# Performance work log

Measured on AMD Instinct MI355X. Metric: run time of the kernel, lower is better.

## Reference

```python
import jax, jax.numpy as jnp
import numpy as np


def l2norm(x, axis=-1, eps=1e-06):
    inv_norm = jax.lax.rsqrt(jnp.sum(x * x, axis=axis, keepdims=True) + eps)
    return x * inv_norm


def setup_inputs() -> dict:
    key0 = jax.random.key(0)
    ks = jax.random.split(key0, 5)
    B, S, H, Dk, Dv = 4, 2048, 16, 128, 128
    query = jax.random.normal(ks[0], (B, S, H, Dk), dtype=jnp.float32)
    key = jax.random.normal(ks[1], (B, S, H, Dk), dtype=jnp.float32)
    value = jax.random.normal(ks[2], (B, S, H, Dv), dtype=jnp.float32)
    # g is a log-decay: negative so decay = exp(g) in (exp(-1), 1)
    g = -jax.random.uniform(ks[3], (B, S, H), dtype=jnp.float32)
    # beta plays the role of sigmoid(.) mixing coefficient in (0, 1)
    beta = jax.random.uniform(ks[4], (B, S, H), dtype=jnp.float32)
    return {"query": query, "key": key, "value": value, "g": g, "beta": beta}


def reference(query, key, value, g, beta):
    # Gated delta-rule recurrence (Qwen3.5 GatedDeltaNet / recurrent_gated_delta_rule)
    dtype = query.dtype
    q = l2norm(query)
    k = l2norm(key)
    v = value
    scale = 1.0 / float(np.sqrt(q.shape[-1]))
    q = q * scale
    # time-major: [S, B, H, D]
    q = jnp.swapaxes(q, 0, 1)
    k = jnp.swapaxes(k, 0, 1)
    v = jnp.swapaxes(v, 0, 1)
    g_t = jnp.swapaxes(g, 0, 1)
    b_t = jnp.swapaxes(beta, 0, 1)
    B, H, Dk = q.shape[1], q.shape[2], q.shape[3]
    Dv = v.shape[3]
    init_state = jnp.zeros((B, H, Dk, Dv), dtype=dtype)

    def step_fn(state, inputs):
        q_i, k_i, v_i, g_i, beta_i = inputs
        decay = jnp.exp(g_i)[..., None, None]            # [B,H,1,1]
        state = state * decay                            # [B,H,Dk,Dv]
        kv_mem = jnp.sum(state * k_i[..., :, None], axis=-2)   # [B,H,Dv]
        delta = (v_i - kv_mem) * beta_i[..., None]              # [B,H,Dv]
        state = state + k_i[..., :, None] * delta[..., None, :]
        out_i = jnp.sum(state * q_i[..., :, None], axis=-2)    # [B,H,Dv]
        return state, out_i

    final_state, outputs = jax.lax.scan(step_fn, init_state, (q, k, v, g_t, b_t))
    outputs = jnp.swapaxes(outputs, 0, 1).astype(dtype)  # [B,S,H,Dv]
    return outputs, final_state.astype(dtype)
```

## Files before the change

kernel.cpp:

```cpp
#include <hip/hip_runtime.h>


#define Bsz 4
#define Ssz 2048
#define Hsz 16
#define Dsz 128

constexpr int ROWS = Bsz * Ssz * Hsz;
constexpr int VSTR = Hsz * Dsz;
constexpr float EPS = 1e-6f;
constexpr float SCALE = 0.08838834764831845f;

typedef float v2f __attribute__((ext_vector_type(2)));

template <int CTRL>
__device__ __forceinline__ float dpp_add(float x) {
  int y = __builtin_amdgcn_update_dpp(0, __float_as_int(x), CTRL, 0xF, 0xF, true);
  return x + __int_as_float(y);
}
__device__ __forceinline__ float reduce16(float x) {
  x = dpp_add<0xB1>(x);
  x = dpp_add<0x4E>(x);
  x = dpp_add<0x141>(x);
  x = dpp_add<0x140>(x);
  return x;
}

__global__ __launch_bounds__(256) void prep_kernel(
    const float* __restrict__ q, const float* __restrict__ k,
    const float* __restrict__ g, const float* __restrict__ beta,
    float4* __restrict__ pack) {
  int wid = threadIdx.x >> 6;
  int lane = threadIdx.x & 63;
  int lg = lane & 15;
  int rg = lane >> 4;
  int r = blockIdx.x * 16 + wid * 4 + rg;
  const float4* qp = reinterpret_cast<const float4*>(q + (size_t)r * Dsz);
  const float4* kp = reinterpret_cast<const float4*>(k + (size_t)r * Dsz);
  float4 qa = qp[lg * 2], qb = qp[lg * 2 + 1];
  float4 ka = kp[lg * 2], kb = kp[lg * 2 + 1];
  float sq = qa.x * qa.x + qa.y * qa.y + qa.z * qa.z + qa.w * qa.w +
             qb.x * qb.x + qb.y * qb.y + qb.z * qb.z + qb.w * qb.w;
  float sk = ka.x * ka.x + ka.y * ka.y + ka.z * ka.z + ka.w * ka.w +
             kb.x * kb.x + kb.y * kb.y + kb.z * kb.z + kb.w * kb.w;
  sq = reduce16(sq);
  sk = reduce16(sk);
  if (lg == 0) {
    float xq = sq + EPS;
    float rq = rsqrtf(xq);
    rq = rq * (1.5f - 0.5f * xq * rq * rq);
    float xk = sk + EPS;
    float rk = rsqrtf(xk);
    rk = rk * (1.5f - 0.5f * xk * rk * rk);
    float dec = expf(g[r]);
    float bi = beta[r] * rk;
    int h = r % Hsz;
    int s = (r / Hsz) % Ssz;
    int b = r / (Hsz * Ssz);
    pack[(size_t)(b * Hsz + h) * Ssz + s] = make_float4(dec, rk, rq * SCALE, bi);
  }
}

#define DDEPTH 8
#define BATCH 4
#define SLOT_B 1280
#define WAVE_B (DDEPTH * SLOT_B)

__device__ __forceinline__ void dma16(unsigned long long g, unsigned int l) {
  __builtin_amdgcn_global_load_lds(
      (const __attribute__((address_space(1))) void*)g,
      (__attribute__((address_space(3))) void*)(unsigned long long)l, 16, 0, 0);
}
__device__ __forceinline__ void dma4(unsigned long long g, unsigned int l) {
  __builtin_amdgcn_global_load_lds(
      (const __attribute__((address_space(1))) void*)g,
      (__attribute__((address_space(3))) void*)(unsigned long long)l, 4, 0, 0);
}

struct BufP {
  v2f kr[4];
  v2f qr[4];
  float4 p;
  float vv;
};

__device__ __forceinline__ void ld_buf(BufP& b, const char* slot, int dkl, int dvg) {
  const float4* kp = (const float4*)(slot + dkl * 16);
  float4 k0 = kp[0];
  float4 k1 = kp[16];
  float4 q0 = kp[32];
  float4 q1 = kp[48];
  b.kr[0] = (v2f){k0.x, k0.y};
  b.kr[1] = (v2f){k0.z, k0.w};
  b.kr[2] = (v2f){k1.x, k1.y};
  b.kr[3] = (v2f){k1.z, k1.w};
  b.qr[0] = (v2f){q0.x, q0.y};
  b.qr[1] = (v2f){q0.z, q0.w};
  b.qr[2] = (v2f){q1.x, q1.y};
  b.qr[3] = (v2f){q1.z, q1.w};
  b.vv = *(const float*)(slot + 1024 + dvg * 4);
  b.p = *(const float4*)(slot + 1040);
}

__device__ __forceinline__ float step_compute(const BufP& b, v2f (&st)[4]) {
  v2f a0 = st[0] * b.kr[0];
  v2f a1 = st[1] * b.kr[1];
  a0 = __builtin_elementwise_fma(st[2], b.kr[2], a0);
  a1 = __builtin_elementwise_fma(st[3], b.kr[3], a1);
  float acc = (a0.x + a0.y) + (a1.x + a1.y);
  acc = reduce16(acc);
  float dec = b.p.x;
  float kv = acc * dec * b.p.y;
  float dl = (b.vv - kv) * b.p.w;
  v2f dec2 = (v2f){dec, dec};
  v2f dl2 = (v2f){dl, dl};
  v2f o0 = (v2f){0.f, 0.f};
  v2f o1 = (v2f){0.f, 0.f};
#pragma unroll
  for (int i = 0; i < 4; i += 2) {
    st[i] = __builtin_elementwise_fma(st[i], dec2, b.kr[i] * dl2);
    st[i + 1] = __builtin_elementwise_fma(st[i + 1], dec2, b.kr[i + 1] * dl2);
    o0 = __builtin_elementwise_fma(st[i], b.qr[i], o0);
    o1 = __builtin_elementwise_fma(st[i + 1], b.qr[i + 1], o1);
  }
  float oacc = (o0.x + o0.y) + (o1.x + o1.y);
  oacc = reduce16(oacc);
  return oacc * b.p.z;
}

__global__ __launch_bounds__(256, 2) void scan_kernel(
    const float* __restrict__ q, const float* __restrict__ k,
    const float* __restrict__ v, const float4* __restrict__ pack,
    float* __restrict__ out, float* __restrict__ stateOut) {
  __shared__ __align__(16) char smem[4 * WAVE_B];

  const int blk = blockIdx.x;
  const int bh = blk & 63;
  const int cc = blk >> 6;
  const int tid = threadIdx.x;
  const int lane = tid & 63;
  const int wid = __builtin_amdgcn_readfirstlane(tid >> 6);
  const int dkl = lane & 15;
  const int dvg = lane >> 4;
  const int dv = cc * 16 + wid * 4 + dvg;

  const size_t base = ((size_t)(bh >> 4) * Ssz * Hsz + (bh & 15)) * Dsz;
  const float4* pp = pack + (size_t)bh * Ssz;

  const unsigned int wb3 =
      (unsigned int)(unsigned long long)(void*)smem + (unsigned int)(wid * WAVE_B);
  const char* wbg = smem + wid * WAVE_B;

  const int li = lane & 31;
  const int fofs = (li < 16) ? (8 * li) : (8 * (li - 16) + 4);
  unsigned long long kq_g =
      (unsigned long long)(uintptr_t)(((lane < 32) ? k : q) + base + fofs);
  unsigned long long vp_g;
  unsigned int vp_stride;
  if (lane < 4) {
    vp_g = (unsigned long long)(uintptr_t)(v + base + cc * 16 + wid * 4 + lane);
    vp_stride = VSTR * 4;
  } else {
    int pc = (lane < 8) ? (lane - 4) : 0;
    vp_g = (unsigned long long)(uintptr_t)((const float*)pp + pc);
    vp_stride = 16;
  }

#pragma unroll
  for (int r = 0; r < DDEPTH; ++r) {
    dma16(kq_g, wb3 + r * SLOT_B);
    dma4(vp_g, wb3 + r * SLOT_B + 1024);
    kq_g += VSTR * 4;
    vp_g += vp_stride;
  }
  int nrow = DDEPTH;

  v2f st[4];
#pragma unroll
  for (int i = 0; i < 4; ++i) st[i] = (v2f){0.f, 0.f};

  float* outp = out + base + (size_t)dkl * VSTR + dv;
  float ocap = 0.f;
  BufP A, Bb;

  for (int sb = 0; sb < Ssz; sb += 16) {
#pragma unroll
    for (int gg = 0; gg < 4; ++gg) {
      const int s0 = (gg & 1) * BATCH;
      asm volatile("s_waitcnt vmcnt(8)" ::: "memory");
      ld_buf(A, wbg + (s0 + 0) * SLOT_B, dkl, dvg);
      __builtin_amdgcn_sched_barrier(0);
      ld_buf(Bb, wbg + (s0 + 1) * SLOT_B, dkl, dvg);
      __builtin_amdgcn_sched_barrier(0);
      {
        float o = step_compute(A, st);
        ocap = (dkl == gg * 4 + 0) ? o : ocap;
      }
      ld_buf(A, wbg + (s0 + 2) * SLOT_B, dkl, dvg);
      __builtin_amdgcn_sched_barrier(0);
      {
        float o = step_compute(Bb, st);
        ocap = (dkl == gg * 4 + 1) ? o : ocap;
      }
      ld_buf(Bb, wbg + (s0 + 3) * SLOT_B, dkl, dvg);
      __builtin_amdgcn_sched_barrier(0);
      {
        float o = step_compute(A, st);
        ocap = (dkl == gg * 4 + 2) ? o : ocap;
      }
      {
        float o = step_compute(Bb, st);
        ocap = (dkl == gg * 4 + 3) ? o : ocap;
      }
      if (gg == 3) {
        *outp = ocap;
        outp += 16 * VSTR;
      }
      asm volatile("s_waitcnt lgkmcnt(0)" ::: "memory");
#pragma unroll
      for (int j = 0; j < BATCH; ++j) {
        dma16(kq_g, wb3 + (s0 + j) * SLOT_B);
        dma4(vp_g, wb3 + (s0 + j) * SLOT_B + 1024);
        if (nrow < Ssz - 1) {
          kq_g += VSTR * 4;
          vp_g += vp_stride;
          ++nrow;
        }
      }
    }
  }

  float* sp = stateOut + ((size_t)bh * Dsz + dkl * 8) * Dsz + dv;
#pragma unroll
  for (int j = 0; j < 4; ++j) {
    sp[(2 * j) * Dsz] = st[j].x;
    sp[(2 * j + 1) * Dsz] = st[j].y;
  }
}

extern "C" void kernel_launch(void* const* d_in, const int* in_sizes, int n_in,
                              void* d_out, int out_size, void* d_ws, size_t ws_size,
                              hipStream_t stream) {
  const float* q = (const float*)d_in[0];
  const float* k = (const float*)d_in[1];
  const float* v = (const float*)d_in[2];
  const float* g = (const float*)d_in[3];
  const float* beta = (const float*)d_in[4];
  float* out = (float*)d_out;
  float* stateOut = out + (size_t)Bsz * Ssz * Hsz * Dsz;
  float4* pack = (float4*)d_ws;

  prep_kernel<<<ROWS / 16, 256, 0, stream>>>(q, k, g, beta, pack);
  scan_kernel<<<512, 256, 0, stream>>>(q, k, v, pack, out, stateOut);
}
```

Measured before the change: 717.7 us.

## Split state across 32 lanes per column and double scan blocks

Each wave now covers 2 value columns with 32 lanes per column instead of 4 columns with 16 lanes, so every lane holds 4 state elements instead of 8. The grid grows to 1024 blocks with occupancy hint 4, and the LDS slot shrinks. Reductions gain a ds_swizzle step across 32 lanes, and only 8 lanes issue the v/pack DMA. The aim is to shorten the per-step serial chain and raise parallelism, at the cost of an extra cross-lane step per reduction and double the k/q staging traffic per column.

```diff
diff --git a/kernel.cpp b/kernel.cpp
--- a/kernel.cpp
+++ b/kernel.cpp
@@ -24,6 +24,11 @@
   x = dpp_add<0x141>(x);
   x = dpp_add<0x140>(x);
   return x;
+}
+__device__ __forceinline__ float reduce32(float x) {
+  x = reduce16(x);
+  int y = __builtin_amdgcn_ds_swizzle(__float_as_int(x), 0x401F);
+  return x + __int_as_float(y);
 }
 
 __global__ __launch_bounds__(256) void prep_kernel(
@@ -63,7 +68,7 @@
 
 #define DDEPTH 8
 #define BATCH 4
-#define SLOT_B 1280
+#define SLOT_B 1056
 #define WAVE_B (DDEPTH * SLOT_B)
 
 __device__ __forceinline__ void dma16(unsigned long long g, unsigned int l) {
@@ -77,58 +82,42 @@
       (__attribute__((address_space(3))) void*)(unsigned long long)l, 4, 0, 0);
 }
 
-struct BufP {
-  v2f kr[4];
-  v2f qr[4];
+struct Buf2 {
+  v2f kr0, kr1, qr0, qr1;
   float4 p;
   float vv;
 };
 
-__device__ __forceinline__ void ld_buf(BufP& b, const char* slot, int dkl, int dvg) {
-  const float4* kp = (const float4*)(slot + dkl * 16);
-  float4 k0 = kp[0];
-  float4 k1 = kp[16];
-  float4 q0 = kp[32];
-  float4 q1 = kp[48];
-  b.kr[0] = (v2f){k0.x, k0.y};
-  b.kr[1] = (v2f){k0.z, k0.w};
-  b.kr[2] = (v2f){k1.x, k1.y};
-  b.kr[3] = (v2f){k1.z, k1.w};
-  b.qr[0] = (v2f){q0.x, q0.y};
-  b.qr[1] = (v2f){q0.z, q0.w};
-  b.qr[2] = (v2f){q1.x, q1.y};
-  b.qr[3] = (v2f){q1.z, q1.w};
-  b.vv = *(const float*)(slot + 1024 + dvg * 4);
+__device__ __forceinline__ void ld_buf2(Buf2& b, const char* slot, int dkl, int dvg) {
+  const float* sf = (const float*)slot;
+  b.kr0 = (v2f){sf[dkl], sf[dkl + 32]};
+  b.kr1 = (v2f){sf[dkl + 64], sf[dkl + 96]};
+  b.qr0 = (v2f){sf[128 + dkl], sf[128 + dkl + 32]};
+  b.qr1 = (v2f){sf[128 + dkl + 64], sf[128 + dkl + 96]};
+  b.vv = sf[256 + dvg];
   b.p = *(const float4*)(slot + 1040);
 }
 
-__device__ __forceinline__ float step_compute(const BufP& b, v2f (&st)[4]) {
-  v2f a0 = st[0] * b.kr[0];
-  v2f a1 = st[1] * b.kr[1];
-  a0 = __builtin_elementwise_fma(st[2], b.kr[2], a0);
-  a1 = __builtin_elementwise_fma(st[3], b.kr[3], a1);
-  float acc = (a0.x + a0.y) + (a1.x + a1.y);
-  acc = reduce16(acc);
+__device__ __forceinline__ float step_compute2(const Buf2& b, v2f (&st)[2]) {
+  v2f a = st[0] * b.kr0;
+  a = __builtin_elementwise_fma(st[1], b.kr1, a);
+  float acc = a.x + a.y;
+  acc = reduce32(acc);
   float dec = b.p.x;
   float kv = acc * dec * b.p.y;
   float dl = (b.vv - kv) * b.p.w;
   v2f dec2 = (v2f){dec, dec};
   v2f dl2 = (v2f){dl, dl};
-  v2f o0 = (v2f){0.f, 0.f};
-  v2f o1 = (v2f){0.f, 0.f};
-#pragma unroll
-  for (int i = 0; i < 4; i += 2) {
-    st[i] = __builtin_elementwise_fma(st[i], dec2, b.kr[i] * dl2);
-    st[i + 1] = __builtin_elementwise_fma(st[i + 1], dec2, b.kr[i + 1] * dl2);
-    o0 = __builtin_elementwise_fma(st[i], b.qr[i], o0);
-    o1 = __builtin_elementwise_fma(st[i + 1], b.qr[i + 1], o1);
-  }
-  float oacc = (o0.x + o0.y) + (o1.x + o1.y);
-  oacc = reduce16(oacc);
+  st[0] = __builtin_elementwise_fma(st[0], dec2, b.kr0 * dl2);
+  st[1] = __builtin_elementwise_fma(st[1], dec2, b.kr1 * dl2);
+  v2f o = st[0] * b.qr0;
+  o = __builtin_elementwise_fma(st[1], b.qr1, o);
+  float oacc = o.x + o.y;
+  oacc = reduce32(oacc);
   return oacc * b.p.z;
 }
 
-__global__ __launch_bounds__(256, 2) void scan_kernel(
+__global__ __launch_bounds__(256, 4) void scan_kernel(
     const float* __restrict__ q, const float* __restrict__ k,
     const float* __restrict__ v, const float4* __restrict__ pack,
     float* __restrict__ out, float* __restrict__ stateOut) {
@@ -140,9 +129,10 @@
   const int tid = threadIdx.x;
   const int lane = tid & 63;
   const int wid = __builtin_amdgcn_readfirstlane(tid >> 6);
-  const int dkl = lane & 15;
-  const int dvg = lane >> 4;
-  const int dv = cc * 16 + wid * 4 + dvg;
+  const int dkl = lane & 31;
+  const int dvg = lane >> 5;
+  const int dv0 = cc * 8 + wid * 2;
+  const int dv = dv0 + dvg;
 
   const size_t base = ((size_t)(bh >> 4) * Ssz * Hsz + (bh & 15)) * Dsz;
   const float4* pp = pack + (size_t)bh * Ssz;
@@ -152,16 +142,15 @@
   const char* wbg = smem + wid * WAVE_B;
 
   const int li = lane & 31;
-  const int fofs = (li < 16) ? (8 * li) : (8 * (li - 16) + 4);
   unsigned long long kq_g =
-      (unsigned long long)(uintptr_t)(((lane < 32) ? k : q) + base + fofs);
+      (unsigned long long)(uintptr_t)(((lane < 32) ? k : q) + base + 4 * li);
   unsigned long long vp_g;
   unsigned int vp_stride;
-  if (lane < 4) {
-    vp_g = (unsigned long long)(uintptr_t)(v + base + cc * 16 + wid * 4 + lane);
+  if (lane < 2) {
+    vp_g = (unsigned long long)(uintptr_t)(v + base + dv0 + lane);
     vp_stride = VSTR * 4;
   } else {
-    int pc = (lane < 8) ? (lane - 4) : 0;
+    int pc = (lane >= 4 && lane < 8) ? (lane - 4) : 0;
     vp_g = (unsigned long long)(uintptr_t)((const float*)pp + pc);
     vp_stride = 16;
   }
@@ -169,58 +158,58 @@
 #pragma unroll
   for (int r = 0; r < DDEPTH; ++r) {
     dma16(kq_g, wb3 + r * SLOT_B);
-    dma4(vp_g, wb3 + r * SLOT_B + 1024);
+    if (lane < 8) dma4(vp_g, wb3 + r * SLOT_B + 1024);
     kq_g += VSTR * 4;
     vp_g += vp_stride;
   }
   int nrow = DDEPTH;
 
-  v2f st[4];
-#pragma unroll
-  for (int i = 0; i < 4; ++i) st[i] = (v2f){0.f, 0.f};
+  v2f st[2];
+  st[0] = (v2f){0.f, 0.f};
+  st[1] = (v2f){0.f, 0.f};
 
   float* outp = out + base + (size_t)dkl * VSTR + dv;
   float ocap = 0.f;
-  BufP A, Bb;
-
-  for (int sb = 0; sb < Ssz; sb += 16) {
+  Buf2 A, Bb;
+
+  for (int sb = 0; sb < Ssz; sb += 32) {
 #pragma unroll
-    for (int gg = 0; gg < 4; ++gg) {
+    for (int gg = 0; gg < 8; ++gg) {
       const int s0 = (gg & 1) * BATCH;
       asm volatile("s_waitcnt vmcnt(8)" ::: "memory");
-      ld_buf(A, wbg + (s0 + 0) * SLOT_B, dkl, dvg);
-      __builtin_amdgcn_sched_barrier(0);
-      ld_buf(Bb, wbg + (s0 + 1) * SLOT_B, dkl, dvg);
-      __builtin_amdgcn_sched_barrier(0);
-      {
-        float o = step_compute(A, st);
+      ld_buf2(A, wbg + (s0 + 0) * SLOT_B, dkl, dvg);
+      __builtin_amdgcn_sched_barrier(0);
+      ld_buf2(Bb, wbg + (s0 + 1) * SLOT_B, dkl, dvg);
+      __builtin_amdgcn_sched_barrier(0);
+      {
+        float o = step_compute2(A, st);
         ocap = (dkl == gg * 4 + 0) ? o : ocap;
       }
-      ld_buf(A, wbg + (s0 + 2) * SLOT_B, dkl, dvg);
-      __builtin_amdgcn_sched_barrier(0);
-      {
-        float o = step_compute(Bb, st);
+      ld_buf2(A, wbg + (s0 + 2) * SLOT_B, dkl, dvg);
+      __builtin_amdgcn_sched_barrier(0);
+      {
+        float o = step_compute2(Bb, st);
         ocap = (dkl == gg * 4 + 1) ? o : ocap;
       }
-      ld_buf(Bb, wbg + (s0 + 3) * SLOT_B, dkl, dvg);
-      __builtin_amdgcn_sched_barrier(0);
-      {
-        float o = step_compute(A, st);
+      ld_buf2(Bb, wbg + (s0 + 3) * SLOT_B, dkl, dvg);
+      __builtin_amdgcn_sched_barrier(0);
+      {
+        float o = step_compute2(A, st);
         ocap = (dkl == gg * 4 + 2) ? o : ocap;
       }
       {
-        float o = step_compute(Bb, st);
+        float o = step_compute2(Bb, st);
         ocap = (dkl == gg * 4 + 3) ? o : ocap;
       }
-      if (gg == 3) {
+      if (gg == 7) {
         *outp = ocap;
-        outp += 16 * VSTR;
+        outp += 32 * VSTR;
       }
       asm volatile("s_waitcnt lgkmcnt(0)" ::: "memory");
 #pragma unroll
       for (int j = 0; j < BATCH; ++j) {
         dma16(kq_g, wb3 + (s0 + j) * SLOT_B);
-        dma4(vp_g, wb3 + (s0 + j) * SLOT_B + 1024);
+        if (lane < 8) dma4(vp_g, wb3 + (s0 + j) * SLOT_B + 1024);
         if (nrow < Ssz - 1) {
           kq_g += VSTR * 4;
           vp_g += vp_stride;
@@ -230,12 +219,11 @@
     }
   }
 
-  float* sp = stateOut + ((size_t)bh * Dsz + dkl * 8) * Dsz + dv;
-#pragma unroll
-  for (int j = 0; j < 4; ++j) {
-    sp[(2 * j) * Dsz] = st[j].x;
-    sp[(2 * j + 1) * Dsz] = st[j].y;
-  }
+  float* sp = stateOut + ((size_t)bh * Dsz + dkl) * Dsz + dv;
+  sp[0 * 32 * Dsz] = st[0].x;
+  sp[1 * 32 * Dsz] = st[0].y;
+  sp[2 * 32 * Dsz] = st[1].x;
+  sp[3 * 32 * Dsz] = st[1].y;
 }
 
 extern "C" void kernel_launch(void* const* d_in, const int* in_sizes, int n_in,
@@ -251,5 +239,5 @@
   float4* pack = (float4*)d_ws;
 
   prep_kernel<<<ROWS / 16, 256, 0, stream>>>(q, k, g, beta, pack);
-  scan_kernel<<<512, 256, 0, stream>>>(q, k, v, pack, out, stateOut);
-}
+  scan_kernel<<<1024, 256, 0, stream>>>(q, k, v, pack, out, stateOut);
+}
```

After: 1.083 ms. +50.9%, slower.
